# Kernel tuning notes

Measured on AMD Instinct MI355X. Metric: run time of the kernel, lower is better.

The kernel has to match this reference:

```python
import jax, jax.numpy as jnp
import numpy as np

HID = 1024
HEADS = 16
HEAD_DIM = HID // HEADS


def setup_inputs() -> dict:
    key = jax.random.key(0)
    ks = jax.random.split(key, 12)
    B, S = 4, 2048
    scale = 0.02
    return {
        "query": jax.random.normal(ks[0], (B, S, HID), jnp.float32),
        "key": jax.random.normal(ks[1], (B, S, HID), jnp.float32),
        "value": jax.random.normal(ks[2], (B, S, HID), jnp.float32),
        "wq": jax.random.normal(ks[3], (HID, HID), jnp.float32) * scale,
        "bq": jnp.zeros((HID,), jnp.float32),
        "wk": jax.random.normal(ks[4], (HID, HID), jnp.float32) * scale,
        "bk": jnp.zeros((HID,), jnp.float32),
        "wv": jax.random.normal(ks[5], (HID, HID), jnp.float32) * scale,
        "bv": jnp.zeros((HID,), jnp.float32),
        "wf": jax.random.normal(ks[6], (HID, HID), jnp.float32) * scale,
        "bf": jnp.zeros((HID,), jnp.float32),
    }


def reference(query, key, value, wq, bq, wk, bk, wv, bv, wf, bf):
    B, S, _ = query.shape
    # torch Linear: y = x @ W.T + b
    Q = (query @ wq.T + bq).reshape(B, S, HEADS, HEAD_DIM).transpose(0, 2, 1, 3)
    K = (key @ wk.T + bk).reshape(B, S, HEADS, HEAD_DIM).transpose(0, 2, 1, 3)
    V = (value @ wv.T + bv).reshape(B, S, HEADS, HEAD_DIM).transpose(0, 2, 1, 3)
    scale = jnp.sqrt(jnp.float32(HEAD_DIM))
    energy = jnp.einsum('bhqd,bhkd->bhqk', Q, K) / scale  # [B,H,S,S]
    attention = jax.nn.softmax(energy, axis=-1)  # dropout p=0 -> identity
    x = jnp.einsum('bhqk,bhkd->bhqd', attention, V)
    x = x.transpose(0, 2, 1, 3).reshape(B, S, HID)
    return x @ wf.T + bf
```

## Files before the change

### kernel.cpp

```cpp
#include <hip/hip_runtime.h>
#include <stdint.h>

#define SEQ 2048
#define HIDDEN 1024
#define NHEADS 16
#define HDIM 64
#define MTOT 8192

#define C1SCALE 0.1803368801111437f

typedef __bf16 bf16x8 __attribute__((ext_vector_type(8)));
typedef unsigned short u16x8 __attribute__((ext_vector_type(8)));
typedef short s16x4 __attribute__((ext_vector_type(4)));
typedef unsigned int u32x4 __attribute__((ext_vector_type(4)));
typedef float f32x4 __attribute__((ext_vector_type(4)));

#define GAS __attribute__((address_space(1)))
#define LAS __attribute__((address_space(3)))

__device__ __forceinline__ unsigned short bf16_rne(float f) {
  union { float f; unsigned int u; } v; v.f = f;
  return (unsigned short)((v.u + 0x7fffu + ((v.u >> 16) & 1u)) >> 16);
}

__device__ __forceinline__ unsigned int pk2(float lo, float hi) {
  unsigned int a = __builtin_bit_cast(unsigned int, hi) + 0x8000u;
  unsigned int b = __builtin_bit_cast(unsigned int, lo) + 0x8000u;
  return __builtin_amdgcn_perm(a, b, 0x07060302u);
}

__device__ __forceinline__ s16x4 pack4_bf16(float a, float b, float c, float d) {
  s16x4 r;
  r[0] = (short)bf16_rne(a); r[1] = (short)bf16_rne(b);
  r[2] = (short)bf16_rne(c); r[3] = (short)bf16_rne(d);
  return r;
}

__device__ __forceinline__ void gload_lds16(const unsigned short* g, unsigned short* l) {
  __builtin_amdgcn_global_load_lds((GAS void*)(unsigned short*)g, (LAS void*)l, 16, 0, 0);
}

__global__ __launch_bounds__(256) void cvt3(const float* __restrict__ a,
                                            const float* __restrict__ b,
                                            const float* __restrict__ c,
                                            unsigned short* __restrict__ out,
                                            int perSeg) {
  const int seg = blockIdx.y;
  const float* in = seg == 0 ? a : (seg == 1 ? b : c);
  int i = blockIdx.x * 256 + threadIdx.x;
  float4 v = ((const float4*)in)[i];
  ushort4 o;
  o.x = bf16_rne(v.x); o.y = bf16_rne(v.y);
  o.z = bf16_rne(v.z); o.w = bf16_rne(v.w);
  ((ushort4*)(out + (size_t)seg * perSeg))[i] = o;
}

__global__ __launch_bounds__(256) void cvt4(const float* __restrict__ a,
                                            const float* __restrict__ b,
                                            const float* __restrict__ c,
                                            const float* __restrict__ d,
                                            unsigned short* __restrict__ out,
                                            int perSeg) {
  const int seg = blockIdx.y;
  const float* in = seg == 0 ? a : (seg == 1 ? b : (seg == 2 ? c : d));
  const float sc = (seg == 0) ? C1SCALE : 1.0f;
  int i = blockIdx.x * 256 + threadIdx.x;
  float4 v = ((const float4*)in)[i];
  ushort4 o;
  o.x = bf16_rne(v.x * sc); o.y = bf16_rne(v.y * sc);
  o.z = bf16_rne(v.z * sc); o.w = bf16_rne(v.w * sc);
  ((ushort4*)(out + (size_t)seg * perSeg))[i] = o;
}

__global__ __launch_bounds__(256) void gemm_qkv(const unsigned short* __restrict__ Xq,
                                                const unsigned short* __restrict__ Xk,
                                                const unsigned short* __restrict__ Xv,
                                                const unsigned short* __restrict__ W,
                                                const float* __restrict__ bq,
                                                const float* __restrict__ bk,
                                                const float* __restrict__ bv,
                                                unsigned short* __restrict__ Qb,
                                                unsigned short* __restrict__ Kb,
                                                unsigned short* __restrict__ Vb) {
  __shared__ unsigned short As[128 * 32];
  __shared__ unsigned short Bs[128 * 32];
  const int tid = threadIdx.x;
  const int lane = tid & 63, w = tid >> 6;
  const int quad = lane >> 4, ln = lane & 15;
  const int wm = w & 1, wn = w >> 1;
  const int mBase = blockIdx.y * 128, nBase = blockIdx.x * 128;
  const int seg = blockIdx.x >> 3;
  const unsigned short* A = seg == 0 ? Xq : (seg == 1 ? Xk : Xv);
  const float* bias = seg == 0 ? bq : (seg == 1 ? bk : bv);
  const float bscale = seg == 0 ? C1SCALE : 1.0f;
  unsigned short* outp = seg == 0 ? Qb : (seg == 1 ? Kb : Vb);
  const int K = HIDDEN;

  f32x4 acc[4][4];
  f32x4 zero = {0.f, 0.f, 0.f, 0.f};
#pragma unroll
  for (int i = 0; i < 4; i++)
#pragma unroll
    for (int j = 0; j < 4; j++) acc[i][j] = zero;

  const int e0 = tid * 8;
  const int e1 = (256 + tid) * 8;
  const int r0 = e0 >> 5, c0 = e0 & 31;
  const int r1 = e1 >> 5, c1 = e1 & 31;
  const unsigned short* Ap0 = A + (size_t)(mBase + r0) * K + c0;
  const unsigned short* Ap1 = A + (size_t)(mBase + r1) * K + c1;
  const unsigned short* Wp0 = W + (size_t)(nBase + r0) * K + c0;
  const unsigned short* Wp1 = W + (size_t)(nBase + r1) * K + c1;

  for (int k0 = 0; k0 < K; k0 += 32) {
    gload_lds16(Ap0 + k0, &As[e0]);
    gload_lds16(Ap1 + k0, &As[e1]);
    gload_lds16(Wp0 + k0, &Bs[e0]);
    gload_lds16(Wp1 + k0, &Bs[e1]);
    __syncthreads();
    u16x8 af[4], bfr[4];
#pragma unroll
    for (int mi = 0; mi < 4; mi++)
      af[mi] = *(const u16x8*)&As[(wm * 64 + mi * 16 + ln) * 32 + quad * 8];
#pragma unroll
    for (int ni = 0; ni < 4; ni++)
      bfr[ni] = *(const u16x8*)&Bs[(wn * 64 + ni * 16 + ln) * 32 + quad * 8];
#pragma unroll
    for (int mi = 0; mi < 4; mi++)
#pragma unroll
      for (int ni = 0; ni < 4; ni++)
        acc[mi][ni] = __builtin_amdgcn_mfma_f32_16x16x32_bf16(
            __builtin_bit_cast(bf16x8, af[mi]), __builtin_bit_cast(bf16x8, bfr[ni]),
            acc[mi][ni], 0, 0, 0);
    __syncthreads();
  }

#pragma unroll
  for (int ni = 0; ni < 4; ni++) {
    const int colg = nBase + wn * 64 + ni * 16 + ln;
    const int col = colg & 1023;
    const float bvv = bias[col] * bscale;
#pragma unroll
    for (int mi = 0; mi < 4; mi++) {
      const int row = mBase + wm * 64 + mi * 16 + quad * 4;
#pragma unroll
      for (int r = 0; r < 4; r++)
        outp[(size_t)(row + r) * HIDDEN + col] = bf16_rne(acc[mi][ni][r] + bvv);
    }
  }
}

__global__ __launch_bounds__(256) void gemm_f(const unsigned short* __restrict__ A,
                                              const unsigned short* __restrict__ W,
                                              const float* __restrict__ bias,
                                              float* __restrict__ Cv) {
  __shared__ unsigned short As[128 * 32];
  __shared__ unsigned short Bs[128 * 32];
  const int tid = threadIdx.x;
  const int lane = tid & 63, w = tid >> 6;
  const int quad = lane >> 4, ln = lane & 15;
  const int wm = w & 1, wn = w >> 1;
  const int mBase = blockIdx.y * 128, nBase = blockIdx.x * 128;
  const int K = HIDDEN, N = HIDDEN;

  f32x4 acc[4][4];
  f32x4 zero = {0.f, 0.f, 0.f, 0.f};
#pragma unroll
  for (int i = 0; i < 4; i++)
#pragma unroll
    for (int j = 0; j < 4; j++) acc[i][j] = zero;

  const int e0 = tid * 8;
  const int e1 = (256 + tid) * 8;
  const int r0 = e0 >> 5, c0 = e0 & 31;
  const int r1 = e1 >> 5, c1 = e1 & 31;
  const unsigned short* Ap0 = A + (size_t)(mBase + r0) * K + c0;
  const unsigned short* Ap1 = A + (size_t)(mBase + r1) * K + c1;
  const unsigned short* Wp0 = W + (size_t)(nBase + r0) * K + c0;
  const unsigned short* Wp1 = W + (size_t)(nBase + r1) * K + c1;

  for (int k0 = 0; k0 < K; k0 += 32) {
    gload_lds16(Ap0 + k0, &As[e0]);
    gload_lds16(Ap1 + k0, &As[e1]);
    gload_lds16(Wp0 + k0, &Bs[e0]);
    gload_lds16(Wp1 + k0, &Bs[e1]);
    __syncthreads();
    u16x8 af[4], bfr[4];
#pragma unroll
    for (int mi = 0; mi < 4; mi++)
      af[mi] = *(const u16x8*)&As[(wm * 64 + mi * 16 + ln) * 32 + quad * 8];
#pragma unroll
    for (int ni = 0; ni < 4; ni++)
      bfr[ni] = *(const u16x8*)&Bs[(wn * 64 + ni * 16 + ln) * 32 + quad * 8];
#pragma unroll
    for (int mi = 0; mi < 4; mi++)
#pragma unroll
      for (int ni = 0; ni < 4; ni++)
        acc[mi][ni] = __builtin_amdgcn_mfma_f32_16x16x32_bf16(
            __builtin_bit_cast(bf16x8, af[mi]), __builtin_bit_cast(bf16x8, bfr[ni]),
            acc[mi][ni], 0, 0, 0);
    __syncthreads();
  }

#pragma unroll
  for (int ni = 0; ni < 4; ni++) {
    const int col = nBase + wn * 64 + ni * 16 + ln;
    const float bvv = bias[col];
#pragma unroll
    for (int mi = 0; mi < 4; mi++) {
      const int row = mBase + wm * 64 + mi * 16 + quad * 4;
#pragma unroll
      for (int r = 0; r < 4; r++)
        Cv[(size_t)(row + r) * N + col] = acc[mi][ni][r] + bvv;
    }
  }
}

__global__ __launch_bounds__(256) void transpose_v(const unsigned short* __restrict__ Vb,
                                                   unsigned short* __restrict__ Vt) {
  __shared__ unsigned short L[128 * 90];
  const int t = blockIdx.x;
  const int bh = t >> 4, kt = t & 15;
  const int b = bh >> 4, h = bh & 15;
  const int tid = threadIdx.x;
  {
    const int key = tid >> 1, hf = tid & 1;
    const unsigned short* src =
        Vb + ((size_t)(b * SEQ + kt * 128 + key)) * HIDDEN + h * HDIM + hf * 32;
    u16x8 a0 = *(const u16x8*)(src);
    u16x8 a1 = *(const u16x8*)(src + 8);
    u16x8 a2 = *(const u16x8*)(src + 16);
    u16x8 a3 = *(const u16x8*)(src + 24);
    unsigned short* dst = &L[key * 90 + hf * 32];
    *(u16x8*)(dst) = a0;
    *(u16x8*)(dst + 8) = a1;
    *(u16x8*)(dst + 16) = a2;
    *(u16x8*)(dst + 24) = a3;
  }
  __syncthreads();
  const int lane = tid & 63, w = tid >> 6;
  const int quad = lane >> 4, ln = lane & 15;
  unsigned short* out = Vt + (size_t)t * 8192;
#pragma unroll
  for (int gg = 0; gg < 4; gg++) {
    const int f = w * 4 + gg;
    const int g = f >> 2, mtd = f & 3;
    u16x8 v;
#pragma unroll
    for (int j = 0; j < 8; j++) {
      const int key = g * 32 + (j >> 2) * 16 + quad * 4 + (j & 3);
      v[j] = L[key * 90 + mtd * 16 + ln];
    }
    *(u16x8*)(out + f * 512 + lane * 8) = v;
  }
}

__global__ __launch_bounds__(256, 4) void attn6(const unsigned short* __restrict__ Q,
                                                const unsigned short* __restrict__ K,
                                                const unsigned short* __restrict__ Vt,
                                                unsigned short* __restrict__ X) {
  const int tid = threadIdx.x, lane = tid & 63, w = tid >> 6;
  const int quad = lane >> 4, ln = lane & 15;
  const int bh = blockIdx.x, b = bh >> 4, h = bh & 15;
  const size_t base = (size_t)b * SEQ * HIDDEN + (size_t)h * HDIM;
  const unsigned short* Qh = Q + base;
  const unsigned short* Kh = K + base;
  const unsigned short* vtile = Vt + (size_t)bh * 16 * 8192;
  const int qw = blockIdx.y * 128 + w * 32;

  u16x8 qf[2][2];
#pragma unroll
  for (int nt = 0; nt < 2; nt++)
#pragma unroll
    for (int kk2 = 0; kk2 < 2; kk2++)
      qf[nt][kk2] = *(const u16x8*)(Qh + (size_t)(qw + nt * 16 + ln) * HIDDEN + kk2 * 32 + quad * 8);

  f32x4 o[4][2];
  f32x4 zero = {0.f, 0.f, 0.f, 0.f};
#pragma unroll
  for (int mtd = 0; mtd < 4; mtd++)
#pragma unroll
    for (int nt = 0; nt < 2; nt++) o[mtd][nt] = zero;
  f32x4 l2[2] = {zero, zero};

  u16x8 onesf;
#pragma unroll
  for (int j = 0; j < 8; j++) onesf[j] = 0x3F80;

  const unsigned short* Kl = Kh + (size_t)ln * HIDDEN + quad * 8;

  u16x8 kp[2][2];
  kp[0][0] = *(const u16x8*)(Kl);
  kp[0][1] = *(const u16x8*)(Kl + 32);
  kp[1][0] = *(const u16x8*)(Kl + 16 * HIDDEN);
  kp[1][1] = *(const u16x8*)(Kl + 16 * HIDDEN + 32);

  for (int kt = 0; kt < 16; ++kt) {
#pragma unroll
    for (int g = 0; g < 4; g++) {
      u16x8 vp[4];
#pragma unroll
      for (int mtd = 0; mtd < 4; mtd++)
        vp[mtd] = *(const u16x8*)(vtile + kt * 8192 + (g * 4 + mtd) * 512 + lane * 8);

      u32x4 P[2];
#pragma unroll
      for (int half = 0; half < 2; half++) {
        const int mt = 2 * g + half;
        const int slot = mt & 1;
        f32x4 s0 = zero, s1 = zero;
        __builtin_amdgcn_s_setprio(1);
        s0 = __builtin_amdgcn_mfma_f32_16x16x32_bf16(
            __builtin_bit_cast(bf16x8, kp[slot][0]), __builtin_bit_cast(bf16x8, qf[0][0]), s0, 0, 0, 0);
        s0 = __builtin_amdgcn_mfma_f32_16x16x32_bf16(
            __builtin_bit_cast(bf16x8, kp[slot][1]), __builtin_bit_cast(bf16x8, qf[0][1]), s0, 0, 0, 0);
        s1 = __builtin_amdgcn_mfma_f32_16x16x32_bf16(
            __builtin_bit_cast(bf16x8, kp[slot][0]), __builtin_bit_cast(bf16x8, qf[1][0]), s1, 0, 0, 0);
        s1 = __builtin_amdgcn_mfma_f32_16x16x32_bf16(
            __builtin_bit_cast(bf16x8, kp[slot][1]), __builtin_bit_cast(bf16x8, qf[1][1]), s1, 0, 0, 0);
        __builtin_amdgcn_s_setprio(0);
        const int nxt = kt * 8 + mt + 2;
        if (nxt < 128) {
          const unsigned short* ka = Kl + (size_t)nxt * 16 * HIDDEN;
          kp[slot][0] = *(const u16x8*)(ka);
          kp[slot][1] = *(const u16x8*)(ka + 32);
        }
        float e0[4], e1[4];
#pragma unroll
        for (int r = 0; r < 4; r++) {
          e0[r] = __builtin_exp2f(s0[r]);
          e1[r] = __builtin_exp2f(s1[r]);
        }
        if (half == 0) {
          P[0][0] = pk2(e0[0], e0[1]); P[0][1] = pk2(e0[2], e0[3]);
          P[1][0] = pk2(e1[0], e1[1]); P[1][1] = pk2(e1[2], e1[3]);
        } else {
          P[0][2] = pk2(e0[0], e0[1]); P[0][3] = pk2(e0[2], e0[3]);
          P[1][2] = pk2(e1[0], e1[1]); P[1][3] = pk2(e1[2], e1[3]);
        }
      }
      __builtin_amdgcn_s_setprio(1);
#pragma unroll
      for (int nt = 0; nt < 2; nt++) {
        bf16x8 pb = __builtin_bit_cast(bf16x8, P[nt]);
        l2[nt] = __builtin_amdgcn_mfma_f32_16x16x32_bf16(
            __builtin_bit_cast(bf16x8, onesf), pb, l2[nt], 0, 0, 0);
#pragma unroll
        for (int mtd = 0; mtd < 4; mtd++)
          o[mtd][nt] = __builtin_amdgcn_mfma_f32_16x16x32_bf16(
              __builtin_bit_cast(bf16x8, vp[mtd]), pb, o[mtd][nt], 0, 0, 0);
      }
      __builtin_amdgcn_s_setprio(0);
    }
  }

  float inv[2];
#pragma unroll
  for (int nt = 0; nt < 2; nt++) inv[nt] = 1.0f / l2[nt][0];

#pragma unroll
  for (int nt = 0; nt < 2; nt++) {
    unsigned short* dst = X + (size_t)(b * SEQ + qw + nt * 16 + ln) * HIDDEN + h * HDIM;
#pragma unroll
    for (int mtd = 0; mtd < 4; mtd++) {
      s16x4 ov = pack4_bf16(o[mtd][nt][0] * inv[nt], o[mtd][nt][1] * inv[nt],
                            o[mtd][nt][2] * inv[nt], o[mtd][nt][3] * inv[nt]);
      *(s16x4*)(dst + mtd * 16 + quad * 4) = ov;
    }
  }
}

extern "C" void kernel_launch(void* const* d_in, const int* in_sizes, int n_in,
                              void* d_out, int out_size, void* d_ws, size_t ws_size,
                              hipStream_t stream) {
  const float* q_in = (const float*)d_in[0];
  const float* k_in = (const float*)d_in[1];
  const float* v_in = (const float*)d_in[2];
  const float* wq = (const float*)d_in[3];
  const float* bq = (const float*)d_in[4];
  const float* wk = (const float*)d_in[5];
  const float* bk = (const float*)d_in[6];
  const float* wv = (const float*)d_in[7];
  const float* bv = (const float*)d_in[8];
  const float* wf = (const float*)d_in[9];
  const float* bfb = (const float*)d_in[10];

  const size_t NX = (size_t)MTOT * HIDDEN;
  const size_t NW = (size_t)HIDDEN * HIDDEN;
  unsigned short* A = (unsigned short*)d_ws;
  unsigned short* Bx = A + NX;
  unsigned short* C = Bx + NX;
  unsigned short* W4 = C + NX;
  unsigned short* Qb = W4 + 4 * NW;
  unsigned short* Kb = Qb + NX;
  unsigned short* Vb = Kb + NX;

  cvt3<<<dim3(NX / 1024, 3), 256, 0, stream>>>(q_in, k_in, v_in, A, (int)NX);
  cvt4<<<dim3(NW / 1024, 4), 256, 0, stream>>>(wq, wk, wv, wf, W4, (int)NW);

  gemm_qkv<<<dim3(24, MTOT / 128), 256, 0, stream>>>(A, Bx, C, W4, bq, bk, bv, Qb, Kb, Vb);
  transpose_v<<<1024, 256, 0, stream>>>(Vb, Bx);
  attn6<<<dim3(NHEADS * 4, SEQ / 128), 256, 0, stream>>>(Qb, Kb, Bx, C);
  gemm_f<<<dim3(8, MTOT / 128), 256, 0, stream>>>(C, W4 + 3 * NW, bfb, (float*)d_out);
}
```

Baseline: 431.3 us.

## Stage K tiles in double-buffered swizzled LDS and prefetch V one group ahead

Each attention block now loads its 128-key K tile into LDS through direct global-to-LDS loads, with an XOR swizzle and double buffering across key tiles. Previously every wave read K separately from global memory. V fragments are also prefetched one group ahead into alternating register sets, so the loads overlap the MFMA work. This removes redundant per-wave K traffic from global memory at the cost of 32KB of LDS per block, which may reduce occupancy, and adds a barrier per key tile.

```diff
diff --git a/kernel.cpp b/kernel.cpp
--- a/kernel.cpp
+++ b/kernel.cpp
@@ -255,10 +255,11 @@
   }
 }
 
-__global__ __launch_bounds__(256, 4) void attn6(const unsigned short* __restrict__ Q,
+__global__ __launch_bounds__(256, 4) void attn7(const unsigned short* __restrict__ Q,
                                                 const unsigned short* __restrict__ K,
                                                 const unsigned short* __restrict__ Vt,
                                                 unsigned short* __restrict__ X) {
+  __shared__ unsigned short Ks[2][128 * 64];
   const int tid = threadIdx.x, lane = tid & 63, w = tid >> 6;
   const int quad = lane >> 4, ln = lane & 15;
   const int bh = blockIdx.x, b = bh >> 4, h = bh & 15;
@@ -268,6 +269,12 @@
   const unsigned short* vtile = Vt + (size_t)bh * 16 * 8192;
   const int qw = blockIdx.y * 128 + w * 32;
 
+  const int kr0 = tid >> 3, kcb = tid & 7;
+  const unsigned short* ksrc = Kh + (size_t)kr0 * HIDDEN + ((kcb ^ (kr0 & 7)) * 8);
+
+  const int krd0 = ln * 64 + ((quad ^ (ln & 7)) * 8);
+  const int krd1 = ln * 64 + (((4 | quad) ^ (ln & 7)) * 8);
+
   u16x8 qf[2][2];
 #pragma unroll
   for (int nt = 0; nt < 2; nt++)
@@ -287,44 +294,59 @@
 #pragma unroll
   for (int j = 0; j < 8; j++) onesf[j] = 0x3F80;
 
-  const unsigned short* Kl = Kh + (size_t)ln * HIDDEN + quad * 8;
-
-  u16x8 kp[2][2];
-  kp[0][0] = *(const u16x8*)(Kl);
-  kp[0][1] = *(const u16x8*)(Kl + 32);
-  kp[1][0] = *(const u16x8*)(Kl + 16 * HIDDEN);
-  kp[1][1] = *(const u16x8*)(Kl + 16 * HIDDEN + 32);
+  u16x8 vA[4], vB[4];
+
+  {
+    unsigned short* kd = &Ks[0][tid * 8];
+    gload_lds16(ksrc, kd);
+    gload_lds16(ksrc + 32 * HIDDEN, kd + 2048);
+    gload_lds16(ksrc + 64 * HIDDEN, kd + 4096);
+    gload_lds16(ksrc + 96 * HIDDEN, kd + 6144);
+  }
+#pragma unroll
+  for (int mtd = 0; mtd < 4; mtd++)
+    vA[mtd] = *(const u16x8*)(vtile + mtd * 512 + lane * 8);
 
   for (int kt = 0; kt < 16; ++kt) {
+    __syncthreads();
+    const unsigned short* kb = &Ks[kt & 1][0];
+    const unsigned short* vt = vtile + kt * 8192;
 #pragma unroll
     for (int g = 0; g < 4; g++) {
-      u16x8 vp[4];
-#pragma unroll
-      for (int mtd = 0; mtd < 4; mtd++)
-        vp[mtd] = *(const u16x8*)(vtile + kt * 8192 + (g * 4 + mtd) * 512 + lane * 8);
-
+      if (g < 3) {
+#pragma unroll
+        for (int mtd = 0; mtd < 4; mtd++) {
+          u16x8 v_ = *(const u16x8*)(vt + ((g + 1) * 4 + mtd) * 512 + lane * 8);
+          if (g & 1) vA[mtd] = v_; else vB[mtd] = v_;
+        }
+      } else if (kt < 15) {
+#pragma unroll
+        for (int mtd = 0; mtd < 4; mtd++)
+          vA[mtd] = *(const u16x8*)(vt + 8192 + mtd * 512 + lane * 8);
+        const unsigned short* ks = ksrc + (size_t)(kt + 1) * (128 * HIDDEN);
+        unsigned short* kd = &Ks[(kt + 1) & 1][tid * 8];
+        gload_lds16(ks, kd);
+        gload_lds16(ks + 32 * HIDDEN, kd + 2048);
+        gload_lds16(ks + 64 * HIDDEN, kd + 4096);
+        gload_lds16(ks + 96 * HIDDEN, kd + 6144);
+      }
       u32x4 P[2];
 #pragma unroll
       for (int half = 0; half < 2; half++) {
         const int mt = 2 * g + half;
-        const int slot = mt & 1;
+        const u16x8 kf0 = *(const u16x8*)&kb[mt * 1024 + krd0];
+        const u16x8 kf1 = *(const u16x8*)&kb[mt * 1024 + krd1];
         f32x4 s0 = zero, s1 = zero;
         __builtin_amdgcn_s_setprio(1);
         s0 = __builtin_amdgcn_mfma_f32_16x16x32_bf16(
-            __builtin_bit_cast(bf16x8, kp[slot][0]), __builtin_bit_cast(bf16x8, qf[0][0]), s0, 0, 0, 0);
+            __builtin_bit_cast(bf16x8, kf0), __builtin_bit_cast(bf16x8, qf[0][0]), s0, 0, 0, 0);
         s0 = __builtin_amdgcn_mfma_f32_16x16x32_bf16(
-            __builtin_bit_cast(bf16x8, kp[slot][1]), __builtin_bit_cast(bf16x8, qf[0][1]), s0, 0, 0, 0);
+            __builtin_bit_cast(bf16x8, kf1), __builtin_bit_cast(bf16x8, qf[0][1]), s0, 0, 0, 0);
         s1 = __builtin_amdgcn_mfma_f32_16x16x32_bf16(
-            __builtin_bit_cast(bf16x8, kp[slot][0]), __builtin_bit_cast(bf16x8, qf[1][0]), s1, 0, 0, 0);
+            __builtin_bit_cast(bf16x8, kf0), __builtin_bit_cast(bf16x8, qf[1][0]), s1, 0, 0, 0);
         s1 = __builtin_amdgcn_mfma_f32_16x16x32_bf16(
-            __builtin_bit_cast(bf16x8, kp[slot][1]), __builtin_bit_cast(bf16x8, qf[1][1]), s1, 0, 0, 0);
+            __builtin_bit_cast(bf16x8, kf1), __builtin_bit_cast(bf16x8, qf[1][1]), s1, 0, 0, 0);
         __builtin_amdgcn_s_setprio(0);
-        const int nxt = kt * 8 + mt + 2;
-        if (nxt < 128) {
-          const unsigned short* ka = Kl + (size_t)nxt * 16 * HIDDEN;
-          kp[slot][0] = *(const u16x8*)(ka);
-          kp[slot][1] = *(const u16x8*)(ka + 32);
-        }
         float e0[4], e1[4];
 #pragma unroll
         for (int r = 0; r < 4; r++) {
@@ -346,9 +368,11 @@
         l2[nt] = __builtin_amdgcn_mfma_f32_16x16x32_bf16(
             __builtin_bit_cast(bf16x8, onesf), pb, l2[nt], 0, 0, 0);
 #pragma unroll
-        for (int mtd = 0; mtd < 4; mtd++)
+        for (int mtd = 0; mtd < 4; mtd++) {
+          u16x8 vv = (g & 1) ? vB[mtd] : vA[mtd];
           o[mtd][nt] = __builtin_amdgcn_mfma_f32_16x16x32_bf16(
-              __builtin_bit_cast(bf16x8, vp[mtd]), pb, o[mtd][nt], 0, 0, 0);
+              __builtin_bit_cast(bf16x8, vv), pb, o[mtd][nt], 0, 0, 0);
+        }
       }
       __builtin_amdgcn_s_setprio(0);
     }
@@ -400,6 +424,6 @@
 
   gemm_qkv<<<dim3(24, MTOT / 128), 256, 0, stream>>>(A, Bx, C, W4, bq, bk, bv, Qb, Kb, Vb);
   transpose_v<<<1024, 256, 0, stream>>>(Vb, Bx);
-  attn6<<<dim3(NHEADS * 4, SEQ / 128), 256, 0, stream>>>(Qb, Kb, Bx, C);
+  attn7<<<dim3(NHEADS * 4, SEQ / 128), 256, 0, stream>>>(Qb, Kb, Bx, C);
   gemm_f<<<dim3(8, MTOT / 128), 256, 0, stream>>>(C, W4 + 3 * NW, bfb, (float*)d_out);
 }
```

Result: faster. 397.9 us (-7.7%).
